# Kernel tuning notes

Hardware: AMD Instinct MI355X
Metric: run time of the kernel (lower is better)

The kernel has to match this reference:

```python
import jax, jax.numpy as jnp
import numpy as np

B, L, D, H, W = 32, 1024, 512, 8, 5  # batch, seq, d_model, heads, local_context_length
DK = D // H


def _local_mix(x, W0, b0, w):
    """Sliding-window local-context weighting (faithful to the torch loop version).
    Pads front with w-1 zeros, applies linear (so padded rows become the bias),
    softmax-weights each length-w causal window against the current position,
    and sums the window.  x: [B, L, D] -> [B, L, D]."""
    Bb, Ll, Dd = x.shape
    xp = jnp.pad(x, ((0, 0), (w - 1, 0), (0, 0)))          # [B, L+w-1, D]
    xp = xp @ W0 + b0                                       # linear AFTER pad (padded rows = bias)
    idx = jnp.arange(Ll)[:, None] + jnp.arange(w)[None, :]  # [L, w] window indices into padded seq
    win = xp[:, idx, :]                                     # [B, L, w, D]
    cur = xp[:, w - 1:, :]                                  # [B, L, D] current positions
    scores = jnp.einsum('bld,blwd->blw', cur, win) / jnp.sqrt(jnp.float32(Dd))
    wts = jax.nn.softmax(scores, axis=-1)                   # [B, L, w]
    return jnp.einsum('blw,blwd->bld', wts, win)            # [B, L, D]


def setup_inputs() -> dict:
    rng = jax.random.key(0)
    ks = jax.random.split(rng, 7)
    s = 0.02
    return {
        'query': jax.random.normal(ks[0], (B, L, D), jnp.float32),
        'key':   jax.random.normal(ks[1], (B, L, D), jnp.float32),
        'value': jax.random.normal(ks[2], (B, L, D), jnp.float32),
        'W0':    jax.random.normal(ks[3], (D, D), jnp.float32) * s,
        'b0':    jax.random.normal(ks[4], (D,), jnp.float32) * s,
        'Wout':  jax.random.normal(ks[5], (D, D), jnp.float32) * s,
        'bout':  jax.random.normal(ks[6], (D,), jnp.float32) * s,
    }


def reference(query, key, value, W0, b0, Wout, bout):
    q = _local_mix(query, W0, b0, W).reshape(B, L, H, DK).transpose(0, 2, 1, 3)  # [B,H,L,dk]
    k = _local_mix(key, W0, b0, W).reshape(B, L, H, DK).transpose(0, 2, 1, 3)
    v = (value @ W0 + b0).reshape(B, L, H, DK).transpose(0, 2, 1, 3)
    scores = jnp.einsum('bhqd,bhkd->bhqk', q, k) / jnp.sqrt(jnp.float32(DK))     # [B,H,L,L]
    p = jax.nn.softmax(scores, axis=-1)
    x = jnp.einsum('bhqk,bhkd->bhqd', p, v)
    x = x.transpose(0, 2, 1, 3).reshape(B, L, D)
    return x @ Wout + bout
```

## Files before the change

kernel.cpp:

```cpp
#include <hip/hip_runtime.h>


typedef __attribute__((ext_vector_type(8))) short bf16x8;
typedef __attribute__((ext_vector_type(4))) float f32x4;

#define MFMA16(a, b, c) __builtin_amdgcn_mfma_f32_16x16x32_bf16((a), (b), (c), 0, 0, 0)

static __device__ __forceinline__ float bf2f(unsigned short u) {
  union { unsigned int i; float f; } v; v.i = ((unsigned int)u) << 16; return v.f;
}
static __device__ __forceinline__ unsigned short f2b(float f) {
  union { float fv; unsigned int i; } v; v.fv = f;
  unsigned int u = v.i;
  return (unsigned short)((u + 0x7fffu + ((u >> 16) & 1u)) >> 16);
}
static __device__ __forceinline__ unsigned int cvtpk(float lo, float hi) {
  unsigned int r;
  asm("v_cvt_pk_bf16_f32 %0, %1, %2" : "=v"(r) : "v"(lo), "v"(hi));
  return r;
}
static __device__ __forceinline__ void glds16(const void* g, void* l) {
  __builtin_amdgcn_global_load_lds(
      (const __attribute__((address_space(1))) unsigned int*)g,
      (__attribute__((address_space(3))) unsigned int*)l, 16, 0, 0);
}
static __device__ __forceinline__ void barrier_lgkm() {
  asm volatile("s_waitcnt lgkmcnt(0)" ::: "memory");
  __builtin_amdgcn_s_barrier();
  __builtin_amdgcn_sched_barrier(0);
}

__global__ __launch_bounds__(256) void tcast2_k(const float* __restrict__ s0,
                                                unsigned short* __restrict__ d0,
                                                const float* __restrict__ s1,
                                                unsigned short* __restrict__ d1) {
  int i = blockIdx.x * 256 + threadIdx.x;
  const float* s = s0;
  unsigned short* d = d0;
  if (i >= 262144) { i -= 262144; s = s1; d = d1; }
  int k = i >> 9, n = i & 511;
  d[(size_t)n * 512 + k] = f2b(s[(size_t)k * 512 + n]);
}

template <int AMODE, int OUTMODE>
__device__ __forceinline__ void gemm64(const void* __restrict__ A_,
                                       const unsigned short* __restrict__ BT,
                                       const float* __restrict__ bias,
                                       void* __restrict__ out_, int bm) {
  __shared__ unsigned short As[2][64 * 32];
  __shared__ unsigned short Bs[2][512 * 32];
  const int tid = threadIdx.x;
  const int w = tid >> 6, l = tid & 63;
  const int lg = l >> 4, lr = l & 15;
  const int wr = w >> 2, wc = w & 3;
  const int rowbase = bm * 64;

  const int arow = tid >> 2, akq = tid & 3;
  const int aslot = (akq ^ ((arow >> 1) & 3)) << 3;

  f32x4 acc[2][8];
#pragma unroll
  for (int m = 0; m < 2; ++m)
#pragma unroll
    for (int n = 0; n < 8; ++n) acc[m][n] = (f32x4){0.f, 0.f, 0.f, 0.f};

  float4 fa0[2], fa1[2];
  uint4 ba0, ba1;

  auto loadA = [&](int t, float4* df, uint4& db) {
    if constexpr (AMODE == 0) {
      const float* p = (const float*)A_ + (size_t)(rowbase + arow) * 512 + t * 32 + akq * 8;
      df[0] = ((const float4*)p)[0];
      df[1] = ((const float4*)p)[1];
    } else {
      db = *(const uint4*)((const unsigned short*)A_ + (size_t)(rowbase + arow) * 512 + t * 32 + akq * 8);
    }
  };
  auto writeA = [&](int buf, const float4* df, const uint4& db) {
    uint4 u;
    if constexpr (AMODE == 0) {
      u.x = cvtpk(df[0].x, df[0].y); u.y = cvtpk(df[0].z, df[0].w);
      u.z = cvtpk(df[1].x, df[1].y); u.w = cvtpk(df[1].z, df[1].w);
    } else {
      u = db;
    }
    *(uint4*)&As[buf][arow * 32 + aslot] = u;
  };
  auto stageB = [&](int t, int buf) {
#pragma unroll
    for (int j = 0; j < 4; ++j) {
      const int jr = j * 128 + w * 16 + (l >> 2);
      const int g = (l & 3) ^ ((jr >> 1) & 3);
      glds16(BT + (size_t)jr * 512 + t * 32 + g * 8,
             &Bs[buf][(j * 128 + w * 16) * 32]);
    }
  };

  if (w < 4) loadA(0, fa0, ba0);
  stageB(0, 0);
  if (w < 4) {
    writeA(0, fa0, ba0);
    loadA(1, fa1, ba1);
  }
  __syncthreads();

  for (int t = 0; t < 16; ++t) {
    const int cur = t & 1;
    if (t < 15) stageB(t + 1, cur ^ 1);
    if (w < 4 && t < 14) {
      if (cur == 0) loadA(t + 2, fa0, ba0);
      else          loadA(t + 2, fa1, ba1);
    }
    bf16x8 af[2];
#pragma unroll
    for (int m = 0; m < 2; ++m) {
      const int r = wr * 32 + m * 16 + lr;
      af[m] = *(const bf16x8*)&As[cur][r * 32 + ((lg ^ ((r >> 1) & 3)) << 3)];
    }
#pragma unroll
    for (int h = 0; h < 2; ++h) {
      bf16x8 bf[4];
#pragma unroll
      for (int ni = 0; ni < 4; ++ni) {
        const int c = wc * 128 + (h * 4 + ni) * 16 + lr;
        bf[ni] = *(const bf16x8*)&Bs[cur][c * 32 + ((lg ^ ((c >> 1) & 3)) << 3)];
      }
      __builtin_amdgcn_s_setprio(1);
#pragma unroll
      for (int m = 0; m < 2; ++m)
#pragma unroll
        for (int ni = 0; ni < 4; ++ni)
          acc[m][h * 4 + ni] = MFMA16(af[m], bf[ni], acc[m][h * 4 + ni]);
      __builtin_amdgcn_s_setprio(0);
    }
    if (w < 4 && t < 15) {
      if (cur == 0) writeA(1, fa1, ba1);
      else          writeA(0, fa0, ba0);
    }
    __syncthreads();
  }

#pragma unroll
  for (int m = 0; m < 2; ++m)
#pragma unroll
    for (int ni = 0; ni < 8; ++ni) {
      const int grow0 = rowbase + wr * 32 + m * 16 + 4 * lg;
      const int gcol = wc * 128 + ni * 16 + lr;
      const float bs = bias[gcol];
#pragma unroll
      for (int r = 0; r < 4; ++r) {
        float v = acc[m][ni][r] + bs;
        if constexpr (OUTMODE == 0)
          ((unsigned short*)out_)[(size_t)(grow0 + r) * 512 + gcol] = f2b(v);
        else
          ((float*)out_)[(size_t)(grow0 + r) * 512 + gcol] = v;
      }
    }
}

__global__ __launch_bounds__(512, 4) void proj3_k(const float* __restrict__ q,
                                                  const float* __restrict__ k,
                                                  const float* __restrict__ v,
                                                  const unsigned short* __restrict__ W0T,
                                                  const float* __restrict__ b0,
                                                  unsigned short* __restrict__ Pq,
                                                  unsigned short* __restrict__ Pk,
                                                  unsigned short* __restrict__ Pv) {
  const int wg = (blockIdx.x & 7) * 192 + (blockIdx.x >> 3);
  const int t = wg >> 9, rem = wg & 511;
  const float* A = t == 0 ? q : t == 1 ? k : v;
  unsigned short* O = t == 0 ? Pq : t == 1 ? Pk : Pv;
  gemm64<0, 0>(A, W0T, b0, O, rem);
}

__global__ __launch_bounds__(512, 4) void gemmout_k(const unsigned short* __restrict__ A,
                                                    const unsigned short* __restrict__ WoT,
                                                    const float* __restrict__ bout,
                                                    float* __restrict__ out) {
  const int wg = (blockIdx.x & 7) * 64 + (blockIdx.x >> 3);
  gemm64<1, 1>(A, WoT, bout, out, wg);
}

__global__ __launch_bounds__(256) void localmix2_k(const unsigned short* __restrict__ Pq,
                                                   const unsigned short* __restrict__ Pk,
                                                   const float* __restrict__ b0,
                                                   unsigned short* __restrict__ Qm,
                                                   unsigned short* __restrict__ Km) {
  const int w = threadIdx.x >> 6, lane = threadIdx.x & 63;
  const int pp = blockIdx.x * 4 + w;
  const unsigned short* P;
  unsigned short* out;
  float outscale;
  int p;
  if (pp < 32768) { P = Pq; out = Qm; outscale = 0.18033688011112042f; p = pp; }
  else            { P = Pk; out = Km; outscale = 1.0f; p = pp - 32768; }
  const int l = p & 1023;
  const int d0 = lane * 8;

  float win[5][8];
#pragma unroll
  for (int j = 0; j < 5; ++j) {
    const int src = l - 4 + j;
    if (src >= 0) {
      const uint4 v = *(const uint4*)(P + (size_t)(p - 4 + j) * 512 + d0);
      const unsigned short* u = (const unsigned short*)&v;
#pragma unroll
      for (int i = 0; i < 8; ++i) win[j][i] = bf2f(u[i]);
    } else {
      const float4 f0 = *(const float4*)(b0 + d0);
      const float4 f1 = *(const float4*)(b0 + d0 + 4);
      win[j][0] = f0.x; win[j][1] = f0.y; win[j][2] = f0.z; win[j][3] = f0.w;
      win[j][4] = f1.x; win[j][5] = f1.y; win[j][6] = f1.z; win[j][7] = f1.w;
    }
  }
  float s[5];
#pragma unroll
  for (int j = 0; j < 5; ++j) {
    float t = 0.f;
#pragma unroll
    for (int i = 0; i < 8; ++i) t += win[4][i] * win[j][i];
    s[j] = t;
  }
#pragma unroll
  for (int off = 1; off < 64; off <<= 1)
#pragma unroll
    for (int j = 0; j < 5; ++j) s[j] += __shfl_xor(s[j], off, 64);
  const float sc = 0.04419417382415922f;
  float mx = -1e30f;
#pragma unroll
  for (int j = 0; j < 5; ++j) { s[j] *= sc; mx = fmaxf(mx, s[j]); }
  float e[5], sum = 0.f;
#pragma unroll
  for (int j = 0; j < 5; ++j) { e[j] = __expf(s[j] - mx); sum += e[j]; }
  const float inv = 1.f / sum;
  __attribute__((ext_vector_type(8))) unsigned short o;
#pragma unroll
  for (int i = 0; i < 8; ++i) {
    float a = 0.f;
#pragma unroll
    for (int j = 0; j < 5; ++j) a += e[j] * win[j][i];
    o[i] = f2b(a * inv * outscale);
  }
  *(__attribute__((ext_vector_type(8))) unsigned short*)(out + (size_t)p * 512 + d0) = o;
}

__global__ __launch_bounds__(256) void attn_k(const unsigned short* __restrict__ Q,
                                              const unsigned short* __restrict__ K,
                                              const unsigned short* __restrict__ V,
                                              unsigned short* __restrict__ AO) {
  __shared__ unsigned short Ks[2][64 * 64];
  __shared__ unsigned short Vt[2][64 * 64];
  const int tid = threadIdx.x;
  const int w = tid >> 6, l = tid & 63;
  const int lg = l >> 4, lr = l & 15;
  const int wg = (blockIdx.x & 7) * 256 + (blockIdx.x >> 3);
  const int qt = wg & 7, bh = wg >> 3;
  const int h = bh & 7, b = bh >> 3;
  const size_t base = (size_t)(b * 1024) * 512 + h * 64;
  const unsigned short* Qb = Q + base + (size_t)(qt * 128) * 512;
  const unsigned short* Kb = K + base;
  const unsigned short* Vb = V + base;

  bf16x8 qf[2][2];
#pragma unroll
  for (int rb = 0; rb < 2; ++rb)
#pragma unroll
    for (int ks = 0; ks < 2; ++ks)
      qf[rb][ks] = *(const bf16x8*)(Qb + (size_t)(w * 32 + rb * 16 + lr) * 512 + ks * 32 + lg * 8);

  f32x4 acc[2][4];
#pragma unroll
  for (int rb = 0; rb < 2; ++rb)
#pragma unroll
    for (int nb = 0; nb < 4; ++nb) acc[rb][nb] = (f32x4){0.f, 0.f, 0.f, 0.f};
  float lsum[2] = {0.f, 0.f};

  const int sk_row = tid >> 2, sk_seg = tid & 3;
  const int r7 = sk_row & 7;
  const int kp = tid & 31, dg = tid >> 5;
  const int k0v = 2 * kp;
  const int vpos0 = (k0v & 32) + ((k0v >> 2) & 3) * 8 + ((k0v >> 4) & 1) * 4 + (k0v & 3);
  const int vg = vpos0 >> 3, vp = vpos0 & 7;

  uint4 kr0, kr1, vr0, vr1;
  auto loadT = [&](int t) {
    const uint4* ksrc = (const uint4*)(Kb + (size_t)(t * 64 + sk_row) * 512 + sk_seg * 16);
    kr0 = ksrc[0]; kr1 = ksrc[1];
    vr0 = *(const uint4*)(Vb + (size_t)(t * 64 + k0v) * 512 + dg * 8);
    vr1 = *(const uint4*)(Vb + (size_t)(t * 64 + k0v + 1) * 512 + dg * 8);
  };
  auto writeT = [&](int bufi) {
    unsigned short* kd = Ks[bufi];
    unsigned short* vd = Vt[bufi];
    *(uint4*)&kd[sk_row * 64 + (((2 * sk_seg) ^ r7) << 3)] = kr0;
    *(uint4*)&kd[sk_row * 64 + (((2 * sk_seg + 1) ^ r7) << 3)] = kr1;
    const unsigned short* u0 = (const unsigned short*)&vr0;
    const unsigned short* u1 = (const unsigned short*)&vr1;
#pragma unroll
    for (int j = 0; j < 8; ++j) {
      const int d = 8 * dg + j;
      const unsigned int pack = (unsigned int)u0[j] | ((unsigned int)u1[j] << 16);
      *(unsigned int*)&vd[d * 64 + ((vg ^ (d & 7)) << 3) + vp] = pack;
    }
  };

  loadT(0);
  writeT(0);
  loadT(1);
  barrier_lgkm();

  const int swz0 = (lg ^ (lr & 7)) << 3, swz1 = ((4 + lg) ^ (lr & 7)) << 3;

  for (int it = 0; it < 16; ++it) {
    const int cur = it & 1;
    f32x4 sf[2][4];
    __builtin_amdgcn_s_setprio(1);
#pragma unroll
    for (int kb = 0; kb < 4; ++kb) {
      const int krow = (kb * 16 + lr) * 64;
      bf16x8 kf0 = *(const bf16x8*)&Ks[cur][krow + swz0];
      bf16x8 kf1 = *(const bf16x8*)&Ks[cur][krow + swz1];
#pragma unroll
      for (int rb = 0; rb < 2; ++rb) {
        f32x4 z = (f32x4){0.f, 0.f, 0.f, 0.f};
        z = MFMA16(kf0, qf[rb][0], z);
        z = MFMA16(kf1, qf[rb][1], z);
        sf[rb][kb] = z;
      }
    }
    __builtin_amdgcn_s_setprio(0);

    if (it < 15) writeT((it + 1) & 1);
    if (it < 14) loadT(it + 2);

#pragma unroll
    for (int rb = 0; rb < 2; ++rb) {
#pragma unroll
      for (int kb = 0; kb < 4; ++kb)
#pragma unroll
        for (int r = 0; r < 4; ++r)
          sf[rb][kb][r] = __builtin_amdgcn_exp2f(sf[rb][kb][r]);
      float s0 = (sf[rb][0][0] + sf[rb][0][1]) + (sf[rb][0][2] + sf[rb][0][3]);
      float s1 = (sf[rb][1][0] + sf[rb][1][1]) + (sf[rb][1][2] + sf[rb][1][3]);
      float s2 = (sf[rb][2][0] + sf[rb][2][1]) + (sf[rb][2][2] + sf[rb][2][3]);
      float s3 = (sf[rb][3][0] + sf[rb][3][1]) + (sf[rb][3][2] + sf[rb][3][3]);
      lsum[rb] += (s0 + s1) + (s2 + s3);
    }

    union { uint4 d; bf16x8 v; } pa[2][2];
#pragma unroll
    for (int rb = 0; rb < 2; ++rb)
#pragma unroll
      for (int t2 = 0; t2 < 2; ++t2) {
        pa[rb][t2].d.x = cvtpk(sf[rb][2 * t2][0], sf[rb][2 * t2][1]);
        pa[rb][t2].d.y = cvtpk(sf[rb][2 * t2][2], sf[rb][2 * t2][3]);
        pa[rb][t2].d.z = cvtpk(sf[rb][2 * t2 + 1][0], sf[rb][2 * t2 + 1][1]);
        pa[rb][t2].d.w = cvtpk(sf[rb][2 * t2 + 1][2], sf[rb][2 * t2 + 1][3]);
      }

    __builtin_amdgcn_s_setprio(1);
#pragma unroll
    for (int t2 = 0; t2 < 2; ++t2) {
      bf16x8 vf[4];
#pragma unroll
      for (int nb = 0; nb < 4; ++nb) {
        const int vrow = (nb * 16 + lr) * 64;
        vf[nb] = *(const bf16x8*)&Vt[cur][vrow + (((4 * t2 + lg) ^ (lr & 7)) << 3)];
      }
#pragma unroll
      for (int rb = 0; rb < 2; ++rb)
#pragma unroll
        for (int nb = 0; nb < 4; ++nb) acc[rb][nb] = MFMA16(pa[rb][t2].v, vf[nb], acc[rb][nb]);
    }
    __builtin_amdgcn_s_setprio(0);
    if (it < 15) barrier_lgkm();
  }

#pragma unroll
  for (int rb = 0; rb < 2; ++rb) {
    float tsum = lsum[rb];
    tsum += __shfl_xor(tsum, 16, 64);
    tsum += __shfl_xor(tsum, 32, 64);
    const float rec = 1.f / tsum;
    float lv[4];
#pragma unroll
    for (int r = 0; r < 4; ++r) lv[r] = __shfl(rec, lg * 4 + r, 64);
#pragma unroll
    for (int nb = 0; nb < 4; ++nb) {
      const int gcol = nb * 16 + lr;
#pragma unroll
      for (int r = 0; r < 4; ++r) {
        const int grow = qt * 128 + w * 32 + rb * 16 + 4 * lg + r;
        AO[base + (size_t)grow * 512 + gcol] = f2b(acc[rb][nb][r] * lv[r]);
      }
    }
  }
}

extern "C" void kernel_launch(void* const* d_in, const int* in_sizes, int n_in,
                              void* d_out, int out_size, void* d_ws, size_t ws_size,
                              hipStream_t stream) {
  const float* query = (const float*)d_in[0];
  const float* key   = (const float*)d_in[1];
  const float* value = (const float*)d_in[2];
  const float* W0    = (const float*)d_in[3];
  const float* b0    = (const float*)d_in[4];
  const float* Wout  = (const float*)d_in[5];
  const float* bout  = (const float*)d_in[6];
  float* out = (float*)d_out;

  char* ws = (char*)d_ws;
  const size_t PSZ = (size_t)32768 * 512 * 2;
  unsigned short* Pq  = (unsigned short*)(ws);
  unsigned short* Pk  = (unsigned short*)(ws + PSZ);
  unsigned short* Pv  = (unsigned short*)(ws + 2 * PSZ);
  unsigned short* Qm  = (unsigned short*)(ws + 3 * PSZ);
  unsigned short* Km  = (unsigned short*)(ws + 4 * PSZ);
  unsigned short* W0T = (unsigned short*)(ws + 5 * PSZ);
  unsigned short* WoT = (unsigned short*)(ws + 5 * PSZ + 524288);

  tcast2_k<<<2048, 256, 0, stream>>>(W0, W0T, Wout, WoT);
  proj3_k<<<1536, 512, 0, stream>>>(query, key, value, W0T, b0, Pq, Pk, Pv);
  localmix2_k<<<16384, 256, 0, stream>>>(Pq, Pk, b0, Qm, Km);
  attn_k<<<2048, 256, 0, stream>>>(Qm, Km, Pv, Pq );
  gemmout_k<<<512, 512, 0, stream>>>(Pq, WoT, bout, out);
}
```

Baseline: 278.6 us.

## Stage full A tile in LDS once and read B fragments directly from global

```diff
diff --git a/kernel.cpp b/kernel.cpp
--- a/kernel.cpp
+++ b/kernel.cpp
@@ -18,11 +18,6 @@
   unsigned int r;
   asm("v_cvt_pk_bf16_f32 %0, %1, %2" : "=v"(r) : "v"(lo), "v"(hi));
   return r;
-}
-static __device__ __forceinline__ void glds16(const void* g, void* l) {
-  __builtin_amdgcn_global_load_lds(
-      (const __attribute__((address_space(1))) unsigned int*)g,
-      (__attribute__((address_space(3))) unsigned int*)l, 16, 0, 0);
 }
 static __device__ __forceinline__ void barrier_lgkm() {
   asm volatile("s_waitcnt lgkmcnt(0)" ::: "memory");
@@ -43,20 +38,43 @@
 }
 
 template <int AMODE, int OUTMODE>
-__device__ __forceinline__ void gemm64(const void* __restrict__ A_,
-                                       const unsigned short* __restrict__ BT,
-                                       const float* __restrict__ bias,
-                                       void* __restrict__ out_, int bm) {
-  __shared__ unsigned short As[2][64 * 32];
-  __shared__ unsigned short Bs[2][512 * 32];
+__device__ __forceinline__ void gemmK(const void* __restrict__ A_,
+                                      const unsigned short* __restrict__ BT,
+                                      const float* __restrict__ bias,
+                                      void* __restrict__ out_, int bm) {
+  __shared__ unsigned short As[64 * 520];
   const int tid = threadIdx.x;
   const int w = tid >> 6, l = tid & 63;
   const int lg = l >> 4, lr = l & 15;
   const int wr = w >> 2, wc = w & 3;
   const int rowbase = bm * 64;
 
-  const int arow = tid >> 2, akq = tid & 3;
-  const int aslot = (akq ^ ((arow >> 1) & 3)) << 3;
+  if constexpr (AMODE == 0) {
+    const float* Af = (const float*)A_ + (size_t)rowbase * 512;
+    float4 v[16];
+#pragma unroll
+    for (int j = 0; j < 16; ++j) v[j] = ((const float4*)Af)[j * 512 + tid];
+#pragma unroll
+    for (int j = 0; j < 16; ++j) {
+      const int i = j * 512 + tid;
+      const int r = i >> 7, c4 = i & 127;
+      uint2 p;
+      p.x = cvtpk(v[j].x, v[j].y);
+      p.y = cvtpk(v[j].z, v[j].w);
+      *(uint2*)&As[r * 520 + c4 * 4] = p;
+    }
+  } else {
+    const unsigned short* Ab = (const unsigned short*)A_ + (size_t)rowbase * 512;
+    uint4 v[8];
+#pragma unroll
+    for (int j = 0; j < 8; ++j) v[j] = ((const uint4*)Ab)[j * 512 + tid];
+#pragma unroll
+    for (int j = 0; j < 8; ++j) {
+      const int i = j * 512 + tid;
+      const int r = i >> 6, c8 = i & 63;
+      *(uint4*)&As[r * 520 + c8 * 8] = v[j];
+    }
+  }
 
   f32x4 acc[2][8];
 #pragma unroll
@@ -64,80 +82,27 @@
 #pragma unroll
     for (int n = 0; n < 8; ++n) acc[m][n] = (f32x4){0.f, 0.f, 0.f, 0.f};
 
-  float4 fa0[2], fa1[2];
-  uint4 ba0, ba1;
-
-  auto loadA = [&](int t, float4* df, uint4& db) {
-    if constexpr (AMODE == 0) {
-      const float* p = (const float*)A_ + (size_t)(rowbase + arow) * 512 + t * 32 + akq * 8;
-      df[0] = ((const float4*)p)[0];
-      df[1] = ((const float4*)p)[1];
-    } else {
-      db = *(const uint4*)((const unsigned short*)A_ + (size_t)(rowbase + arow) * 512 + t * 32 + akq * 8);
-    }
-  };
-  auto writeA = [&](int buf, const float4* df, const uint4& db) {
-    uint4 u;
-    if constexpr (AMODE == 0) {
-      u.x = cvtpk(df[0].x, df[0].y); u.y = cvtpk(df[0].z, df[0].w);
-      u.z = cvtpk(df[1].x, df[1].y); u.w = cvtpk(df[1].z, df[1].w);
-    } else {
-      u = db;
-    }
-    *(uint4*)&As[buf][arow * 32 + aslot] = u;
-  };
-  auto stageB = [&](int t, int buf) {
-#pragma unroll
-    for (int j = 0; j < 4; ++j) {
-      const int jr = j * 128 + w * 16 + (l >> 2);
-      const int g = (l & 3) ^ ((jr >> 1) & 3);
-      glds16(BT + (size_t)jr * 512 + t * 32 + g * 8,
-             &Bs[buf][(j * 128 + w * 16) * 32]);
-    }
-  };
-
-  if (w < 4) loadA(0, fa0, ba0);
-  stageB(0, 0);
-  if (w < 4) {
-    writeA(0, fa0, ba0);
-    loadA(1, fa1, ba1);
-  }
-  __syncthreads();
-
-  for (int t = 0; t < 16; ++t) {
-    const int cur = t & 1;
-    if (t < 15) stageB(t + 1, cur ^ 1);
-    if (w < 4 && t < 14) {
-      if (cur == 0) loadA(t + 2, fa0, ba0);
-      else          loadA(t + 2, fa1, ba1);
-    }
+  barrier_lgkm();
+
+  const unsigned short* Bw = BT + (size_t)(wc * 128) * 512;
+#pragma unroll 2
+  for (int ks = 0; ks < 16; ++ks) {
+    bf16x8 bf[8];
+#pragma unroll
+    for (int ni = 0; ni < 8; ++ni)
+      bf[ni] = *(const bf16x8*)(Bw + (size_t)(ni * 16 + lr) * 512 + ks * 32 + lg * 8);
     bf16x8 af[2];
 #pragma unroll
     for (int m = 0; m < 2; ++m) {
       const int r = wr * 32 + m * 16 + lr;
-      af[m] = *(const bf16x8*)&As[cur][r * 32 + ((lg ^ ((r >> 1) & 3)) << 3)];
-    }
-#pragma unroll
-    for (int h = 0; h < 2; ++h) {
-      bf16x8 bf[4];
-#pragma unroll
-      for (int ni = 0; ni < 4; ++ni) {
-        const int c = wc * 128 + (h * 4 + ni) * 16 + lr;
-        bf[ni] = *(const bf16x8*)&Bs[cur][c * 32 + ((lg ^ ((c >> 1) & 3)) << 3)];
-      }
-      __builtin_amdgcn_s_setprio(1);
-#pragma unroll
-      for (int m = 0; m < 2; ++m)
-#pragma unroll
-        for (int ni = 0; ni < 4; ++ni)
-          acc[m][h * 4 + ni] = MFMA16(af[m], bf[ni], acc[m][h * 4 + ni]);
-      __builtin_amdgcn_s_setprio(0);
-    }
-    if (w < 4 && t < 15) {
-      if (cur == 0) writeA(1, fa1, ba1);
-      else          writeA(0, fa0, ba0);
-    }
-    __syncthreads();
+      af[m] = *(const bf16x8*)&As[r * 520 + ks * 32 + lg * 8];
+    }
+    __builtin_amdgcn_s_setprio(1);
+#pragma unroll
+    for (int m = 0; m < 2; ++m)
+#pragma unroll
+      for (int ni = 0; ni < 8; ++ni) acc[m][ni] = MFMA16(af[m], bf[ni], acc[m][ni]);
+    __builtin_amdgcn_s_setprio(0);
   }
 
 #pragma unroll
@@ -170,7 +135,7 @@
   const int t = wg >> 9, rem = wg & 511;
   const float* A = t == 0 ? q : t == 1 ? k : v;
   unsigned short* O = t == 0 ? Pq : t == 1 ? Pk : Pv;
-  gemm64<0, 0>(A, W0T, b0, O, rem);
+  gemmK<0, 0>(A, W0T, b0, O, rem);
 }
 
 __global__ __launch_bounds__(512, 4) void gemmout_k(const unsigned short* __restrict__ A,
@@ -178,7 +143,7 @@
                                                     const float* __restrict__ bout,
                                                     float* __restrict__ out) {
   const int wg = (blockIdx.x & 7) * 64 + (blockIdx.x >> 3);
-  gemm64<1, 1>(A, WoT, bout, out, wg);
+  gemmK<1, 1>(A, WoT, bout, out, wg);
 }
 
 __global__ __launch_bounds__(256) void localmix2_k(const unsigned short* __restrict__ Pq,
```

Result: slower. 418.8 us (+50.3%).
